# Kernel optimization log

Hardware: AMD Instinct MI355X
Metric: run time of the kernel (lower is better)

## Reference

```python
import jax, jax.numpy as jnp
import numpy as np


def setup_inputs() -> dict:
    key = jax.random.key(0)
    ks = jax.random.split(key, 5)
    B, S, D, H, K = 2, 2048, 1024, 16, 64
    std = 0.02
    return {
        "x": jax.random.normal(ks[0], (B, S, D), dtype=jnp.float32),
        "W_Q": jax.random.normal(ks[1], (H, D, K), dtype=jnp.float32) * std,
        "W_K": jax.random.normal(ks[2], (H, D, K), dtype=jnp.float32) * std,
        "W_V": jax.random.normal(ks[3], (H, D, K), dtype=jnp.float32) * std,
        "W_O": jax.random.normal(ks[4], (H, K, D), dtype=jnp.float32) * std,
        "b_Q": jnp.zeros((H, K), dtype=jnp.float32),
        "b_K": jnp.zeros((H, K), dtype=jnp.float32),
        "b_V": jnp.zeros((H, K), dtype=jnp.float32),
        "b_O": jnp.zeros((D,), dtype=jnp.float32),
    }


def reference(x, W_Q, W_K, W_V, W_O, b_Q, b_K, b_V, b_O):
    # x: (B, S, D); W_*: (H, D, K); W_O: (H, K, D)
    S = x.shape[1]
    d_head = W_Q.shape[-1]
    q = jnp.einsum('bpd,hdk->bphk', x, W_Q) + b_Q
    k = jnp.einsum('bpd,hdk->bphk', x, W_K) + b_K
    v = jnp.einsum('bpd,hdk->bphk', x, W_V) + b_V
    scores = jnp.einsum('bphk,bqhk->bhpq', q, k) / jnp.sqrt(jnp.float32(d_head))
    # causal mask: positions q > p (strict upper triangle) are masked
    causal = jnp.tril(jnp.ones((S, S), dtype=bool))
    scores = jnp.where(causal, scores, jnp.float32(-jnp.inf))
    pattern = jax.nn.softmax(scores, axis=-1)
    z = jnp.einsum('bhpq,bqhk->bphk', pattern, v)
    out = jnp.einsum('bphk,hkd->bpd', z, W_O) + b_O
    return out
```

## Files before the change

kernel.cpp:

```cpp
#include <hip/hip_runtime.h>

typedef unsigned short u16;
typedef __attribute__((ext_vector_type(4))) float f32x4;
typedef __attribute__((ext_vector_type(8))) short s16x8;
typedef __attribute__((ext_vector_type(4))) unsigned short u16x4;

#define S_ 2048
#define D_ 1024
#define H_ 16
#define KH 64
#define M_ 4096
#define BH_ 32

__device__ __forceinline__ float bf2f(u16 v) {
    union { unsigned int u; float f; } x; x.u = ((unsigned int)v) << 16; return x.f;
}
__device__ __forceinline__ u16 f2bf(float f) {
    union { float ff; unsigned int u; } x; x.ff = f;
    unsigned int r = x.u + 0x7fffu + ((x.u >> 16) & 1u);
    return (u16)(r >> 16);
}

__global__ void kcvt_x(const float* __restrict__ x, u16* __restrict__ xb) {
    const int i = (blockIdx.x * 256 + threadIdx.x) * 4;
    const float4 v = *(const float4*)&x[i];
    u16x4 o;
    o.x = f2bf(v.x); o.y = f2bf(v.y); o.z = f2bf(v.z); o.w = f2bf(v.w);
    *(u16x4*)&xb[i] = o;
}

__global__ void ktrans_w(const float* __restrict__ WQ, const float* __restrict__ WK,
                         const float* __restrict__ WV, const float* __restrict__ WO,
                         u16* __restrict__ wt) {
    __shared__ u16 tile[64][65];
    const int mat = blockIdx.z;
    const float* src = (mat == 0) ? WQ : (mat == 1) ? WK : (mat == 2) ? WV : WO;
    u16* dst = wt + (size_t)mat * 1048576;
    const int a0 = blockIdx.x * 64, b0 = blockIdx.y * 64;
    const int t = threadIdx.x;
    const int bl = t & 63, ar = t >> 6;
    #pragma unroll
    for (int i = 0; i < 16; ++i) {
        int a = a0 + i * 4 + ar, b = b0 + bl;
        size_t sa = (mat < 3) ? (((size_t)(b >> 6)) << 16) + ((size_t)a << 6) + (b & 63)
                              : (size_t)a * 1024 + b;
        tile[i * 4 + ar][bl] = f2bf(src[sa]);
    }
    __syncthreads();
    #pragma unroll
    for (int i = 0; i < 16; ++i) {
        int bl2 = i * 4 + ar;
        dst[(size_t)(b0 + bl2) * 1024 + a0 + bl] = tile[bl][bl2];
    }
}

__global__ void ktrans_v(const u16* __restrict__ V, u16* __restrict__ Vt) {
    __shared__ u16 tile[64][65];
    const int bh = blockIdx.y;
    const int s0 = blockIdx.x * 64;
    const u16* src = V + (size_t)bh * S_ * KH;
    u16* dst = Vt + (size_t)bh * S_ * KH;
    const int t = threadIdx.x, kl = t & 63, sr = t >> 6;
    #pragma unroll
    for (int i = 0; i < 16; ++i)
        tile[i * 4 + sr][kl] = src[(size_t)(s0 + i * 4 + sr) * KH + kl];
    __syncthreads();
    #pragma unroll
    for (int i = 0; i < 16; ++i) {
        int k = i * 4 + sr;
        dst[(size_t)k * S_ + s0 + kl] = tile[kl][k];
    }
}

template <int MODE>
__global__ __launch_bounds__(256)
void kgemm(const u16* __restrict__ A, const u16* __restrict__ Wt,
           const float* __restrict__ b0p, const float* __restrict__ b1p,
           const float* __restrict__ b2p,
           u16* __restrict__ o0, u16* __restrict__ o1, u16* __restrict__ o2,
           float* __restrict__ fo) {
    __shared__ u16 As[2][128 * 32];
    __shared__ u16 Bs[2][128 * 32];
    const int t = threadIdx.x;
    const int l = t & 63, w = t >> 6;
    const int lq = l & 15, lg = l >> 4;
    const int wr = w >> 1, wc = w & 1;
    const int m0 = blockIdx.x * 128;
    const int n0 = blockIdx.y * 128;

    const u16* Bt;
    const float* bias;
    u16* out = nullptr;
    if constexpr (MODE == 0) {
        const int z = blockIdx.z;
        Bt = Wt + (size_t)z * 1048576;
        bias = (z == 0) ? b0p : (z == 1) ? b1p : b2p;
        out = (z == 0) ? o0 : (z == 1) ? o1 : o2;
    } else {
        Bt = Wt; bias = b0p;
    }

    f32x4 acc[4][4] = {};

    auto stage = [&](int kt, int buf) {
        #pragma unroll
        for (int i = 0; i < 2; ++i) {
            int idx = t + i * 256;
            int row = idx >> 2, cc = idx & 3;
            const u16* ga = A + (size_t)(m0 + row) * 1024 + kt * 32 + cc * 8;
            const u16* gb = Bt + (size_t)(n0 + row) * 1024 + kt * 32 + cc * 8;
            __builtin_amdgcn_global_load_lds(
                (const __attribute__((address_space(1))) unsigned int*)ga,
                (__attribute__((address_space(3))) unsigned int*)(&As[buf][idx * 8]),
                16, 0, 0);
            __builtin_amdgcn_global_load_lds(
                (const __attribute__((address_space(1))) unsigned int*)gb,
                (__attribute__((address_space(3))) unsigned int*)(&Bs[buf][idx * 8]),
                16, 0, 0);
        }
    };

    stage(0, 0);
    __syncthreads();
    for (int kt = 0; kt < 32; ++kt) {
        const int cur = kt & 1;
        if (kt + 1 < 32) stage(kt + 1, cur ^ 1);
        s16x8 af[4], bf[4];
        #pragma unroll
        for (int m = 0; m < 4; ++m)
            af[m] = *(const s16x8*)&As[cur][(wr * 64 + m * 16 + lq) * 32 + lg * 8];
        #pragma unroll
        for (int n = 0; n < 4; ++n)
            bf[n] = *(const s16x8*)&Bs[cur][(wc * 64 + n * 16 + lq) * 32 + lg * 8];
        #pragma unroll
        for (int m = 0; m < 4; ++m)
            #pragma unroll
            for (int n = 0; n < 4; ++n)
                acc[m][n] = __builtin_amdgcn_mfma_f32_16x16x32_bf16(
                    af[m], bf[n], acc[m][n], 0, 0, 0);
        __syncthreads();
    }

    #pragma unroll
    for (int n = 0; n < 4; ++n) {
        const int gcol = n0 + wc * 64 + n * 16 + lq;
        const float bv = bias[gcol];
        #pragma unroll
        for (int m = 0; m < 4; ++m) {
            const int growb = m0 + wr * 64 + m * 16 + lg * 4;
            #pragma unroll
            for (int r = 0; r < 4; ++r) {
                const float v = acc[m][n][r] + bv;
                const int grow = growb + r;
                if constexpr (MODE == 0) {
                    const int b = grow >> 11, s = grow & 2047;
                    const int h = gcol >> 6, kk = gcol & 63;
                    out[(((size_t)(b * H_ + h)) * S_ + s) * KH + kk] = f2bf(v);
                } else {
                    fo[(size_t)grow * 1024 + gcol] = v;
                }
            }
        }
    }
}

__global__ __launch_bounds__(256)
void kattn(const u16* __restrict__ Q, const u16* __restrict__ K,
           const u16* __restrict__ Vt, u16* __restrict__ Z) {
    __shared__ u16 Ks[2][64 * 64];
    __shared__ u16 Vs[2][64 * 64];
    __shared__ u16 Pl[4][16 * 72];
    const int t = threadIdx.x, l = t & 63, w = t >> 6;
    const int lq = l & 15, lg = l >> 4;
    const int bh = blockIdx.y, pair = blockIdx.x;
    const size_t base = (size_t)bh * (S_ * KH);
    const u16* Qb = Q + base;
    const u16* Kb = K + base;
    const u16* Vb = Vt + base;
    const int b = bh >> 4, h = bh & 15;
    u16* Pw = &Pl[w][0];

    const int c0 = ((lg ^ (lq & 7)) * 8);
    const int c1 = c0 ^ 32;

    auto stage = [&](int k0, int buf) {
        #pragma unroll
        for (int i = 0; i < 2; ++i) {
            const int idx = t + i * 256;
            const int row = idx >> 3;
            const int cg = (idx & 7) ^ (row & 7);
            __builtin_amdgcn_global_load_lds(
                (const __attribute__((address_space(1))) unsigned int*)
                    (Kb + (size_t)(k0 + row) * KH + cg * 8),
                (__attribute__((address_space(3))) unsigned int*)(&Ks[buf][idx * 8]),
                16, 0, 0);
            __builtin_amdgcn_global_load_lds(
                (const __attribute__((address_space(1))) unsigned int*)
                    (Vb + (size_t)row * S_ + k0 + cg * 8),
                (__attribute__((address_space(3))) unsigned int*)(&Vs[buf][idx * 8]),
                16, 0, 0);
        }
    };

    const float SCL = 0.18033688011112042f;

    #pragma unroll 1
    for (int ph = 0; ph < 2; ++ph) {
        const int qt = ph ? (31 - pair) : pair;
        const int nt = qt + 1;
        const int qs = qt * 64 + w * 16;

        const s16x8 qf0 = *(const s16x8*)&Qb[(size_t)(qs + lq) * KH + lg * 8];
        const s16x8 qf1 = *(const s16x8*)&Qb[(size_t)(qs + lq) * KH + 32 + lg * 8];

        float mrow[4] = {-__builtin_inff(), -__builtin_inff(),
                         -__builtin_inff(), -__builtin_inff()};
        float lrow[4] = {0.f, 0.f, 0.f, 0.f};
        f32x4 zacc[4] = {};

        stage(0, 0);
        __syncthreads();

        for (int kt = 0; kt < nt; ++kt) {
            const int buf = kt & 1;
            const int k0 = kt * 64;
            if (kt + 1 < nt) stage((kt + 1) * 64, buf ^ 1);

            f32x4 sf[4] = {};
            __builtin_amdgcn_s_setprio(1);
            #pragma unroll
            for (int kf = 0; kf < 4; ++kf) {
                const int row = kf * 16 + lq;
                const s16x8 ka = *(const s16x8*)&Ks[buf][row * 64 + c0];
                const s16x8 kb = *(const s16x8*)&Ks[buf][row * 64 + c1];
                sf[kf] = __builtin_amdgcn_mfma_f32_16x16x32_bf16(qf0, ka, sf[kf], 0, 0, 0);
                sf[kf] = __builtin_amdgcn_mfma_f32_16x16x32_bf16(qf1, kb, sf[kf], 0, 0, 0);
            }
            __builtin_amdgcn_s_setprio(0);

            float p[4][4];
            float tmax[4] = {-__builtin_inff(), -__builtin_inff(),
                             -__builtin_inff(), -__builtin_inff()};
            #pragma unroll
            for (int kf = 0; kf < 4; ++kf)
                #pragma unroll
                for (int r = 0; r < 4; ++r) {
                    float v = sf[kf][r] * SCL;
                    if (kt == qt) {
                        const int qg = qs + lg * 4 + r;
                        const int kg = k0 + kf * 16 + lq;
                        if (kg > qg) v = -__builtin_inff();
                    }
                    p[kf][r] = v;
                    tmax[r] = fmaxf(tmax[r], v);
                }
            #pragma unroll
            for (int r = 0; r < 4; ++r) {
                tmax[r] = fmaxf(tmax[r], __shfl_xor(tmax[r], 1));
                tmax[r] = fmaxf(tmax[r], __shfl_xor(tmax[r], 2));
                tmax[r] = fmaxf(tmax[r], __shfl_xor(tmax[r], 4));
                tmax[r] = fmaxf(tmax[r], __shfl_xor(tmax[r], 8));
            }
            float alpha[4], rsum[4];
            #pragma unroll
            for (int r = 0; r < 4; ++r) {
                const float nm = fmaxf(mrow[r], tmax[r]);
                alpha[r] = exp2f(mrow[r] - nm);
                mrow[r] = nm;
                rsum[r] = 0.f;
            }
            #pragma unroll
            for (int kf = 0; kf < 4; ++kf)
                #pragma unroll
                for (int r = 0; r < 4; ++r) {
                    const float e = exp2f(p[kf][r] - mrow[r]);
                    p[kf][r] = e;
                    rsum[r] += e;
                }
            #pragma unroll
            for (int r = 0; r < 4; ++r) {
                rsum[r] += __shfl_xor(rsum[r], 1);
                rsum[r] += __shfl_xor(rsum[r], 2);
                rsum[r] += __shfl_xor(rsum[r], 4);
                rsum[r] += __shfl_xor(rsum[r], 8);
                lrow[r] = lrow[r] * alpha[r] + rsum[r];
            }
            #pragma unroll
            for (int nf = 0; nf < 4; ++nf)
                #pragma unroll
                for (int r = 0; r < 4; ++r)
                    zacc[nf][r] *= alpha[r];

            #pragma unroll
            for (int kf = 0; kf < 4; ++kf)
                #pragma unroll
                for (int r = 0; r < 4; ++r)
                    Pw[(lg * 4 + r) * 72 + kf * 16 + lq] = f2bf(p[kf][r]);
            const s16x8 pa0 = *(const s16x8*)&Pw[lq * 72 + lg * 8];
            const s16x8 pa1 = *(const s16x8*)&Pw[lq * 72 + 32 + lg * 8];

            __builtin_amdgcn_s_setprio(1);
            #pragma unroll
            for (int nf = 0; nf < 4; ++nf) {
                const int row = nf * 16 + lq;
                const s16x8 v0 = *(const s16x8*)&Vs[buf][row * 64 + c0];
                const s16x8 v1 = *(const s16x8*)&Vs[buf][row * 64 + c1];
                zacc[nf] = __builtin_amdgcn_mfma_f32_16x16x32_bf16(pa0, v0, zacc[nf], 0, 0, 0);
                zacc[nf] = __builtin_amdgcn_mfma_f32_16x16x32_bf16(pa1, v1, zacc[nf], 0, 0, 0);
            }
            __builtin_amdgcn_s_setprio(0);
            __syncthreads();
        }

        #pragma unroll
        for (int nf = 0; nf < 4; ++nf)
            #pragma unroll
            for (int r = 0; r < 4; ++r) {
                const float v = zacc[nf][r] / lrow[r];
                const int srow = qs + lg * 4 + r;
                const int col = h * 64 + nf * 16 + lq;
                Z[(size_t)(b * S_ + srow) * 1024 + col] = f2bf(v);
            }
    }
}

extern "C" void kernel_launch(void* const* d_in, const int* in_sizes, int n_in,
                              void* d_out, int out_size, void* d_ws, size_t ws_size,
                              hipStream_t stream) {
    const float* x  = (const float*)d_in[0];
    const float* WQ = (const float*)d_in[1];
    const float* WK = (const float*)d_in[2];
    const float* WV = (const float*)d_in[3];
    const float* WO = (const float*)d_in[4];
    const float* bQ = (const float*)d_in[5];
    const float* bK = (const float*)d_in[6];
    const float* bV = (const float*)d_in[7];
    const float* bO = (const float*)d_in[8];
    float* out = (float*)d_out;

    u16* ws  = (u16*)d_ws;
    u16* xb  = ws;
    u16* wt  = xb + 4194304u;
    u16* Qb  = wt + 4194304u;
    u16* Kb  = Qb + 4194304u;
    u16* Vtb = Kb + 4194304u;
    u16* Zb  = Vtb + 4194304u;
    u16* Vb  = Zb;

    kcvt_x<<<dim3(4096), 256, 0, stream>>>(x, xb);
    ktrans_w<<<dim3(16, 16, 4), 256, 0, stream>>>(WQ, WK, WV, WO, wt);
    kgemm<0><<<dim3(32, 8, 3), 256, 0, stream>>>(
        xb, wt, bQ, bK, bV, Qb, Kb, Vb, nullptr);
    ktrans_v<<<dim3(32, BH_), 256, 0, stream>>>(Vb, Vtb);
    kattn<<<dim3(16, BH_), 256, 0, stream>>>(Qb, Kb, Vtb, Zb);
    kgemm<1><<<dim3(32, 8, 1), 256, 0, stream>>>(
        Zb, wt + 3u * 1048576u, bO, nullptr, nullptr,
        nullptr, nullptr, nullptr, out);
}
```

Before: 238.6 us.

## Transpose QK^T MFMA so each lane owns one query row; lazy softmax rescale

Swaps the MFMA operands so the score tile comes out transposed, giving each lane a single query row. Row max and sum then need only two cross-lane shuffles instead of four per row. The running-max rescale of the accumulators is skipped unless some row's max grows by more than 8 (in log2 units). P is packed with the hardware v_cvt_pk_bf16 instruction and written with vector stores, and the final divide becomes a multiply by a reciprocal. The lazy rescale lets exponentials reach up to 2^8 before renormalising, which slightly changes numerics and adds a wave-wide vote.

After: 215.3 us. 1.11x faster.

```diff
diff --git a/kernel.cpp b/kernel.cpp
--- a/kernel.cpp
+++ b/kernel.cpp
@@ -4,6 +4,7 @@
 typedef __attribute__((ext_vector_type(4))) float f32x4;
 typedef __attribute__((ext_vector_type(8))) short s16x8;
 typedef __attribute__((ext_vector_type(4))) unsigned short u16x4;
+typedef __attribute__((ext_vector_type(2))) unsigned int u32x2;
 
 #define S_ 2048
 #define D_ 1024
@@ -19,6 +20,11 @@
     union { float ff; unsigned int u; } x; x.ff = f;
     unsigned int r = x.u + 0x7fffu + ((x.u >> 16) & 1u);
     return (u16)(r >> 16);
+}
+__device__ __forceinline__ unsigned int cvt_pk_bf16(float lo, float hi) {
+    unsigned int d;
+    asm("v_cvt_pk_bf16_f32 %0, %1, %2" : "=v"(d) : "v"(lo), "v"(hi));
+    return d;
 }
 
 __global__ void kcvt_x(const float* __restrict__ x, u16* __restrict__ xb) {
@@ -182,6 +188,7 @@
 
     const int c0 = ((lg ^ (lq & 7)) * 8);
     const int c1 = c0 ^ 32;
+    const float NINF = -__builtin_inff();
 
     auto stage = [&](int k0, int buf) {
         #pragma unroll
@@ -209,13 +216,13 @@
         const int qt = ph ? (31 - pair) : pair;
         const int nt = qt + 1;
         const int qs = qt * 64 + w * 16;
+        const int lim = w * 16 + lq;
 
         const s16x8 qf0 = *(const s16x8*)&Qb[(size_t)(qs + lq) * KH + lg * 8];
         const s16x8 qf1 = *(const s16x8*)&Qb[(size_t)(qs + lq) * KH + 32 + lg * 8];
 
-        float mrow[4] = {-__builtin_inff(), -__builtin_inff(),
-                         -__builtin_inff(), -__builtin_inff()};
-        float lrow[4] = {0.f, 0.f, 0.f, 0.f};
+        float mrow = NINF;
+        float lrow = 0.f;
         f32x4 zacc[4] = {};
 
         stage(0, 0);
@@ -223,7 +230,6 @@
 
         for (int kt = 0; kt < nt; ++kt) {
             const int buf = kt & 1;
-            const int k0 = kt * 64;
             if (kt + 1 < nt) stage((kt + 1) * 64, buf ^ 1);
 
             f32x4 sf[4] = {};
@@ -233,69 +239,66 @@
                 const int row = kf * 16 + lq;
                 const s16x8 ka = *(const s16x8*)&Ks[buf][row * 64 + c0];
                 const s16x8 kb = *(const s16x8*)&Ks[buf][row * 64 + c1];
-                sf[kf] = __builtin_amdgcn_mfma_f32_16x16x32_bf16(qf0, ka, sf[kf], 0, 0, 0);
-                sf[kf] = __builtin_amdgcn_mfma_f32_16x16x32_bf16(qf1, kb, sf[kf], 0, 0, 0);
+                sf[kf] = __builtin_amdgcn_mfma_f32_16x16x32_bf16(ka, qf0, sf[kf], 0, 0, 0);
+                sf[kf] = __builtin_amdgcn_mfma_f32_16x16x32_bf16(kb, qf1, sf[kf], 0, 0, 0);
             }
             __builtin_amdgcn_s_setprio(0);
 
             float p[4][4];
-            float tmax[4] = {-__builtin_inff(), -__builtin_inff(),
-                             -__builtin_inff(), -__builtin_inff()};
+            const bool diag = (kt == qt);
             #pragma unroll
             for (int kf = 0; kf < 4; ++kf)
                 #pragma unroll
                 for (int r = 0; r < 4; ++r) {
                     float v = sf[kf][r] * SCL;
-                    if (kt == qt) {
-                        const int qg = qs + lg * 4 + r;
-                        const int kg = k0 + kf * 16 + lq;
-                        if (kg > qg) v = -__builtin_inff();
-                    }
+                    if (diag && (kf * 16 + lg * 4 + r) > lim) v = NINF;
                     p[kf][r] = v;
-                    tmax[r] = fmaxf(tmax[r], v);
                 }
-            #pragma unroll
-            for (int r = 0; r < 4; ++r) {
-                tmax[r] = fmaxf(tmax[r], __shfl_xor(tmax[r], 1));
-                tmax[r] = fmaxf(tmax[r], __shfl_xor(tmax[r], 2));
-                tmax[r] = fmaxf(tmax[r], __shfl_xor(tmax[r], 4));
-                tmax[r] = fmaxf(tmax[r], __shfl_xor(tmax[r], 8));
-            }
-            float alpha[4], rsum[4];
-            #pragma unroll
-            for (int r = 0; r < 4; ++r) {
-                const float nm = fmaxf(mrow[r], tmax[r]);
-                alpha[r] = exp2f(mrow[r] - nm);
-                mrow[r] = nm;
-                rsum[r] = 0.f;
-            }
+
+            float mk[4];
             #pragma unroll
             for (int kf = 0; kf < 4; ++kf)
-                #pragma unroll
-                for (int r = 0; r < 4; ++r) {
-                    const float e = exp2f(p[kf][r] - mrow[r]);
-                    p[kf][r] = e;
-                    rsum[r] += e;
-                }
-            #pragma unroll
-            for (int r = 0; r < 4; ++r) {
-                rsum[r] += __shfl_xor(rsum[r], 1);
-                rsum[r] += __shfl_xor(rsum[r], 2);
-                rsum[r] += __shfl_xor(rsum[r], 4);
-                rsum[r] += __shfl_xor(rsum[r], 8);
-                lrow[r] = lrow[r] * alpha[r] + rsum[r];
-            }
-            #pragma unroll
-            for (int nf = 0; nf < 4; ++nf)
+                mk[kf] = fmaxf(fmaxf(p[kf][0], p[kf][1]), fmaxf(p[kf][2], p[kf][3]));
+            float tmax = fmaxf(fmaxf(mk[0], mk[1]), fmaxf(mk[2], mk[3]));
+            tmax = fmaxf(tmax, __shfl_xor(tmax, 16));
+            tmax = fmaxf(tmax, __shfl_xor(tmax, 32));
+
+            float alpha = 1.f;
+            if (!__all(tmax <= mrow + 8.f)) {
+                const float nm = fmaxf(mrow, tmax);
+                alpha = exp2f(mrow - nm);
+                mrow = nm;
+                float alp[4];
                 #pragma unroll
                 for (int r = 0; r < 4; ++r)
-                    zacc[nf][r] *= alpha[r];
-
-            #pragma unroll
-            for (int kf = 0; kf < 4; ++kf)
+                    alp[r] = __shfl(alpha, lg * 4 + r);
+                #pragma unroll
+                for (int nf = 0; nf < 4; ++nf)
+                    #pragma unroll
+                    for (int r = 0; r < 4; ++r)
+                        zacc[nf][r] *= alp[r];
+            }
+
+            float sk[4];
+            #pragma unroll
+            for (int kf = 0; kf < 4; ++kf) {
                 #pragma unroll
                 for (int r = 0; r < 4; ++r)
-                    Pw[(lg * 4 + r) * 72 + kf * 16 + lq] = f2bf(p[kf][r]);
+                    p[kf][r] = exp2f(p[kf][r] - mrow);
+                sk[kf] = (p[kf][0] + p[kf][1]) + (p[kf][2] + p[kf][3]);
+            }
+            float rsum = (sk[0] + sk[1]) + (sk[2] + sk[3]);
+            rsum += __shfl_xor(rsum, 16);
+            rsum += __shfl_xor(rsum, 32);
+            lrow = lrow * alpha + rsum;
+
+            #pragma unroll
+            for (int kf = 0; kf < 4; ++kf) {
+                u32x2 wp;
+                wp.x = cvt_pk_bf16(p[kf][0], p[kf][1]);
+                wp.y = cvt_pk_bf16(p[kf][2], p[kf][3]);
+                *(u32x2*)&Pw[lq * 72 + kf * 16 + lg * 4] = wp;
+            }
             const s16x8 pa0 = *(const s16x8*)&Pw[lq * 72 + lg * 8];
             const s16x8 pa1 = *(const s16x8*)&Pw[lq * 72 + 32 + lg * 8];
 
@@ -312,11 +315,15 @@
             __syncthreads();
         }
 
+        float rinv[4];
+        #pragma unroll
+        for (int r = 0; r < 4; ++r)
+            rinv[r] = 1.f / __shfl(lrow, lg * 4 + r);
         #pragma unroll
         for (int nf = 0; nf < 4; ++nf)
             #pragma unroll
             for (int r = 0; r < 4; ++r) {
-                const float v = zacc[nf][r] / lrow[r];
+                const float v = zacc[nf][r] * rinv[r];
                 const int srow = qs + lg * 4 + r;
                 const int col = h * 64 + nf * 16 + lq;
                 Z[(size_t)(b * S_ + srow) * 1024 + col] = f2bf(v);
```
